# Kernel tuning notes

Hardware: AMD Instinct MI355X
Metric: run time of the kernel (lower is better)

## Reference

```python
import jax, jax.numpy as jnp
import numpy as np
import math

N_HEAD = 16
N_EMBD = 1024
HEAD_DIM = N_EMBD // N_HEAD
B, T = 2, 2048


def setup_inputs() -> dict:
    key = jax.random.key(0)
    k1, k2, k3 = jax.random.split(key, 3)
    scale = 0.02
    x = jax.random.normal(k1, (B, T, N_EMBD), dtype=jnp.float32)
    W_attn = jax.random.normal(k2, (N_EMBD, 3 * N_EMBD), dtype=jnp.float32) * scale
    b_attn = jnp.zeros((3 * N_EMBD,), dtype=jnp.float32)
    W_proj = jax.random.normal(k3, (N_EMBD, N_EMBD), dtype=jnp.float32) * scale
    b_proj = jnp.zeros((N_EMBD,), dtype=jnp.float32)
    return {"x": x, "W_attn": W_attn, "b_attn": b_attn, "W_proj": W_proj, "b_proj": b_proj}


def reference(x, W_attn, b_attn, W_proj, b_proj):
    b, t, c = x.shape
    qkv = x @ W_attn + b_attn                      # [B,T,3C]
    q, k, v = jnp.split(qkv, 3, axis=-1)
    # [B,T,C] -> [B,H,T,D]
    def heads(z):
        return z.reshape(b, t, N_HEAD, HEAD_DIM).transpose(0, 2, 1, 3)
    q, k, v = heads(q), heads(k), heads(v)
    att = jnp.einsum('bhqd,bhkd->bhqk', q, k) * (1.0 / math.sqrt(HEAD_DIM))
    causal = jnp.tril(jnp.ones((t, t), dtype=bool))  # [T,T]
    att = jnp.where(causal[None, None], att, -jnp.inf)
    att = jax.nn.softmax(att, axis=-1)
    y = jnp.einsum('bhqk,bhkd->bhqd', att, v)      # [B,H,T,D]
    y = y.transpose(0, 2, 1, 3).reshape(b, t, c)   # [B,T,C]
    return y @ W_proj + b_proj
```

## Files before the change

### kernel.cpp

```cpp
#include <hip/hip_runtime.h>
#include <hip/hip_bf16.h>


typedef __bf16 bf16_t;
typedef __bf16 bf16x8 __attribute__((ext_vector_type(8)));
typedef float f32x4 __attribute__((ext_vector_type(4)));
typedef unsigned short ushort_t;

#define QSCALE 0.18033688011f

__device__ __forceinline__ void glds16(const bf16_t* g, ushort_t* l) {
  __builtin_amdgcn_global_load_lds(
      (const __attribute__((address_space(1))) unsigned int*)g,
      (__attribute__((address_space(3))) unsigned int*)l, 16, 0, 0);
}

__global__ __launch_bounds__(256) void prep_kernel(
    const float* __restrict__ x, const float* __restrict__ W_attn,
    const float* __restrict__ W_proj, ushort_t* __restrict__ Xb,
    ushort_t* __restrict__ WtA, ushort_t* __restrict__ WtP) {
  const int bid = blockIdx.x, tid = threadIdx.x;
  if (bid < 4096) {
    int i = bid * 256 + tid;
    float4 v = ((const float4*)x)[i];
    ushort4 o;
    o.x = __builtin_bit_cast(unsigned short, (bf16_t)v.x);
    o.y = __builtin_bit_cast(unsigned short, (bf16_t)v.y);
    o.z = __builtin_bit_cast(unsigned short, (bf16_t)v.z);
    o.w = __builtin_bit_cast(unsigned short, (bf16_t)v.w);
    ((ushort4*)Xb)[i] = o;
    return;
  }
  __shared__ ushort_t tile[32][33];
  const float* in;
  ushort_t* out;
  int C, bx, by;
  if (bid < 4096 + 3072) { int idx = bid - 4096; in = W_attn; out = WtA; C = 3072; bx = idx % 96; by = idx / 96; }
  else                   { int idx = bid - 7168; in = W_proj; out = WtP; C = 1024; bx = idx % 32; by = idx / 32; }
  const int tx = tid & 31, ty = tid >> 5;
  int cbase = bx * 32, rbase = by * 32;
#pragma unroll
  for (int i = ty; i < 32; i += 8)
    tile[i][tx] = __builtin_bit_cast(
        unsigned short, (bf16_t)in[(size_t)(rbase + i) * C + cbase + tx]);
  __syncthreads();
#pragma unroll
  for (int i = ty; i < 32; i += 8)
    out[(size_t)(cbase + i) * 1024 + rbase + tx] = tile[tx][i];
}

__device__ __forceinline__ void gemm128_mainloop(
    const bf16_t* __restrict__ A, const bf16_t* __restrict__ Bt, int K,
    int mtile, int ntile, ushort_t* As, ushort_t* Bs, f32x4 acc[4][4]) {
  const int tid  = threadIdx.x;
  const int lane = tid & 63, wave = tid >> 6;
  const int l15  = lane & 15, quad = lane >> 4;
  const int wrow = (wave >> 1) * 64, wcol = (wave & 1) * 64;
  const int lr = lane >> 2;
  const int lc = (((lane & 3) ^ ((lr >> 1) & 3)) * 8);
  const bf16_t* Ap = A + (size_t)(mtile + wave * 32 + lr) * K + lc;
  const bf16_t* Bp = Bt + (size_t)(ntile + wave * 32 + lr) * K + lc;
  const int rsw = (quad ^ ((l15 >> 1) & 3)) * 8;
  ushort_t* Asw = As + wave * 32 * 32;
  ushort_t* Bsw = Bs + wave * 32 * 32;
  for (int kb = 0; kb < K; kb += 32) {
    __syncthreads();
#pragma unroll
    for (int c = 0; c < 2; c++) {
      glds16(Ap + (size_t)(c * 16) * K + kb, Asw + c * 16 * 32);
      glds16(Bp + (size_t)(c * 16) * K + kb, Bsw + c * 16 * 32);
    }
    __syncthreads();
    bf16x8 af[4], bfr[4];
#pragma unroll
    for (int i = 0; i < 4; i++)
      af[i] = *(const bf16x8*)&As[(wrow + i * 16 + l15) * 32 + rsw];
#pragma unroll
    for (int j = 0; j < 4; j++)
      bfr[j] = *(const bf16x8*)&Bs[(wcol + j * 16 + l15) * 32 + rsw];
#pragma unroll
    for (int i = 0; i < 4; i++)
#pragma unroll
      for (int j = 0; j < 4; j++)
        acc[i][j] = __builtin_amdgcn_mfma_f32_16x16x32_bf16(af[i], bfr[j], acc[i][j], 0, 0, 0);
  }
}

__global__ __launch_bounds__(256) void qkv_gemm_kernel(
    const bf16_t* __restrict__ X, const bf16_t* __restrict__ WtA,
    const float* __restrict__ bias, bf16_t* __restrict__ Qd,
    bf16_t* __restrict__ Kd, bf16_t* __restrict__ Vtd) {
  __shared__ ushort_t As[128 * 32];
  __shared__ ushort_t Bs[128 * 32];
  const int mtile = blockIdx.x * 128, ntile = blockIdx.y * 128;
  f32x4 acc[4][4] = {};
  gemm128_mainloop(X, WtA, 1024, mtile, ntile, As, Bs, acc);
  const int tid = threadIdx.x, lane = tid & 63, wave = tid >> 6;
  const int l15 = lane & 15, quad = lane >> 4;
  const int wrow = (wave >> 1) * 64, wcol = (wave & 1) * 64;
#pragma unroll
  for (int j = 0; j < 4; j++) {
    int n = ntile + wcol + j * 16 + l15;
    float bv = bias[n];
    int sec = n >> 10, cc = n & 1023, h = cc >> 6, d = cc & 63;
    float sv = (sec == 0) ? QSCALE : 1.0f;
#pragma unroll
    for (int i = 0; i < 4; i++) {
#pragma unroll
      for (int r = 0; r < 4; r++) {
        int m = mtile + wrow + i * 16 + quad * 4 + r;
        int b = m >> 11, t = m & 2047;
        size_t bh = (size_t)(b * 16 + h);
        bf16_t v = (bf16_t)((acc[i][j][r] + bv) * sv);
        if (sec == 0)      Qd[(bh * 2048 + t) * 64 + d] = v;
        else if (sec == 1) Kd[(bh * 2048 + t) * 64 + d] = v;
        else               Vtd[(bh * 64 + d) * 2048 + t] = v;
      }
    }
  }
}

__global__ __launch_bounds__(512) void attn_kernel(
    const bf16_t* __restrict__ Q, const bf16_t* __restrict__ K,
    const bf16_t* __restrict__ Vt, bf16_t* __restrict__ Y) {
  __shared__ ushort_t Ks[2][4096];
  __shared__ ushort_t Vs[2][4096];
  __shared__ ushort_t Ps[8][16 * 40];
  const int bh = blockIdx.y;
  const int qt = (blockIdx.y < 16) ? (15 - (int)blockIdx.x) : (int)blockIdx.x;
  const int tid = threadIdx.x, wave = tid >> 6, lane = tid & 63;
  const int l15 = lane & 15, quad = lane >> 4;
  const bf16_t* Qh = Q + (size_t)bh * 2048 * 64;
  const bf16_t* Kh = K + (size_t)bh * 2048 * 64;
  const bf16_t* Vh = Vt + (size_t)bh * 64 * 2048;
  const int b = bh >> 4, h = bh & 15;
  const int qw = qt * 128 + wave * 16;
  const int nkt = 2 * qt + 2;

  bf16x8 qa[2];
#pragma unroll
  for (int kc = 0; kc < 2; kc++)
    qa[kc] = *(const bf16x8*)(Qh + (size_t)(qw + l15) * 64 + kc * 32 + quad * 8);

  f32x4 o[4] = {};
  float lpart[4] = {};
  const int rsw = (quad ^ ((l15 >> 1) & 3)) * 8;

  const int lr4 = lane >> 2;
  const int csw = ((lane & 3) ^ ((lr4 >> 1) & 3)) * 8;
  const bool isK = wave < 4;
  const int sw = isK ? wave : wave - 4;
  const int rbase = (sw & 1) * 32;
  const bf16_t* gp0;
  size_t rowstep;
  if (isK) { gp0 = Kh + (size_t)(rbase + lr4) * 64 + (sw >> 1) * 32 + csw;  rowstep = 64; }
  else     { gp0 = Vh + (size_t)(rbase + lr4) * 2048 + (sw >> 1) * 32 + csw; rowstep = 2048; }
  const size_t kstep = isK ? (size_t)64 * 64 : 64;
  ushort_t* dst0 = (isK ? Ks[0] : Vs[0]) + (sw >> 1) * 2048 + rbase * 32;
  ushort_t* dst1 = (isK ? Ks[1] : Vs[1]) + (sw >> 1) * 2048 + rbase * 32;

#pragma unroll
  for (int c = 0; c < 2; c++)
    glds16(gp0 + (size_t)(c * 16) * rowstep, dst0 + c * 512);

  f32x4 zz = {0.f, 0.f, 0.f, 0.f};
  for (int kt = 0; kt < nkt; kt++) {
    const int cur = kt & 1;
    __syncthreads();
    if (kt + 1 < nkt) {
      ushort_t* nd = cur ? dst0 : dst1;
#pragma unroll
      for (int c = 0; c < 2; c++)
        glds16(gp0 + (size_t)(kt + 1) * kstep + (size_t)(c * 16) * rowstep, nd + c * 512);
    }
#pragma unroll
    for (int h32 = 0; h32 < 2; h32++) {
      const int kb32 = kt * 64 + h32 * 32;
      if (kb32 > qw + 15) break;
      bf16x8 kb[2][2];
#pragma unroll
      for (int bn = 0; bn < 2; bn++)
#pragma unroll
        for (int kc = 0; kc < 2; kc++)
          kb[bn][kc] = *(const bf16x8*)&Ks[cur][kc * 2048 + (h32 * 32 + bn * 16 + l15) * 32 + rsw];
      f32x4 s[2];
#pragma unroll
      for (int bn = 0; bn < 2; bn++) {
        f32x4 t0 = __builtin_amdgcn_mfma_f32_16x16x32_bf16(qa[0], kb[bn][0], zz, 0, 0, 0);
        s[bn] = __builtin_amdgcn_mfma_f32_16x16x32_bf16(qa[1], kb[bn][1], t0, 0, 0, 0);
      }
      const bool dg = (kb32 + 31 > qw);
#pragma unroll
      for (int r = 0; r < 4; r++) {
        int row = qw + quad * 4 + r;
        float v0 = s[0][r];
        float v1 = s[1][r];
        if (dg) {
          int c0 = kb32 + l15;
          if (c0 > row) v0 = -1e5f;
          if (c0 + 16 > row) v1 = -1e5f;
        }
        float p0 = __builtin_amdgcn_exp2f(v0);
        float p1 = __builtin_amdgcn_exp2f(v1);
        lpart[r] += p0 + p1;
        int prow = (quad * 4 + r) * 40;
        Ps[wave][prow + l15]      = __builtin_bit_cast(unsigned short, (bf16_t)p0);
        Ps[wave][prow + 16 + l15] = __builtin_bit_cast(unsigned short, (bf16_t)p1);
      }
      bf16x8 vb[4];
#pragma unroll
      for (int ns = 0; ns < 4; ns++)
        vb[ns] = *(const bf16x8*)&Vs[cur][h32 * 2048 + (ns * 16 + l15) * 32 + rsw];
      __asm__ volatile("" ::: "memory");
      bf16x8 pa = *(const bf16x8*)&Ps[wave][l15 * 40 + quad * 8];
#pragma unroll
      for (int ns = 0; ns < 4; ns++)
        o[ns] = __builtin_amdgcn_mfma_f32_16x16x32_bf16(pa, vb[ns], o[ns], 0, 0, 0);
    }
  }
#pragma unroll
  for (int r = 0; r < 4; r++) {
    float l = lpart[r];
#pragma unroll
    for (int off = 1; off < 16; off <<= 1) l += __shfl_xor(l, off);
    float inv_l = 1.0f / fmaxf(l, 1e-30f);
    int t = qw + quad * 4 + r;
#pragma unroll
    for (int ns = 0; ns < 4; ns++) {
      int c = h * 64 + ns * 16 + l15;
      Y[((size_t)(b * 2048 + t)) * 1024 + c] = (bf16_t)(o[ns][r] * inv_l);
    }
  }
}

__global__ __launch_bounds__(256) void proj_gemm_kernel(
    const bf16_t* __restrict__ Yb, const bf16_t* __restrict__ WtP,
    const float* __restrict__ bias, float* __restrict__ out) {
  __shared__ ushort_t As[128 * 32];
  __shared__ ushort_t Bs[64 * 32];
  const int tid = threadIdx.x;
  const int lane = tid & 63, wave = tid >> 6;
  const int l15 = lane & 15, quad = lane >> 4;
  const int wrow = (wave >> 1) * 64, wcol = (wave & 1) * 32;
  const int mtile = blockIdx.x * 128, ntile = blockIdx.y * 64;
  const int K = 1024;
  const int lr = lane >> 2;
  const int lc = (((lane & 3) ^ ((lr >> 1) & 3)) * 8);
  const bf16_t* Ap = Yb + (size_t)(mtile + wave * 32 + lr) * K + lc;
  const bf16_t* Bp = WtP + (size_t)(ntile + wave * 16 + lr) * K + lc;
  const int rsw = (quad ^ ((l15 >> 1) & 3)) * 8;
  ushort_t* Asw = As + wave * 32 * 32;
  ushort_t* Bsw = Bs + wave * 16 * 32;
  f32x4 acc[4][2] = {};
  for (int kb = 0; kb < K; kb += 32) {
    __syncthreads();
    glds16(Ap + kb, Asw);
    glds16(Ap + (size_t)16 * K + kb, Asw + 16 * 32);
    glds16(Bp + kb, Bsw);
    __syncthreads();
    bf16x8 af[4], bfr[2];
#pragma unroll
    for (int i = 0; i < 4; i++)
      af[i] = *(const bf16x8*)&As[(wrow + i * 16 + l15) * 32 + rsw];
#pragma unroll
    for (int j = 0; j < 2; j++)
      bfr[j] = *(const bf16x8*)&Bs[(wcol + j * 16 + l15) * 32 + rsw];
#pragma unroll
    for (int i = 0; i < 4; i++)
#pragma unroll
      for (int j = 0; j < 2; j++)
        acc[i][j] = __builtin_amdgcn_mfma_f32_16x16x32_bf16(af[i], bfr[j], acc[i][j], 0, 0, 0);
  }
  const int tid2 = threadIdx.x;
  (void)tid2;
#pragma unroll
  for (int j = 0; j < 2; j++) {
    int n = ntile + wcol + j * 16 + l15;
    float bv = bias[n];
#pragma unroll
    for (int i = 0; i < 4; i++) {
#pragma unroll
      for (int r = 0; r < 4; r++) {
        int m = mtile + wrow + i * 16 + quad * 4 + r;
        out[(size_t)m * 1024 + n] = acc[i][j][r] + bv;
      }
    }
  }
}

extern "C" void kernel_launch(void* const* d_in, const int* in_sizes, int n_in,
                              void* d_out, int out_size, void* d_ws, size_t ws_size,
                              hipStream_t stream) {
  const float* x      = (const float*)d_in[0];
  const float* W_attn = (const float*)d_in[1];
  const float* b_attn = (const float*)d_in[2];
  const float* W_proj = (const float*)d_in[3];
  const float* b_proj = (const float*)d_in[4];
  float* out = (float*)d_out;

  bf16_t* ws  = (bf16_t*)d_ws;
  bf16_t* WtA = ws;
  bf16_t* WtP = WtA + (size_t)3072 * 1024;
  bf16_t* Xb  = WtP + (size_t)1024 * 1024;
  bf16_t* Qb  = Xb + (size_t)4194304;
  bf16_t* Kb  = Qb + (size_t)4194304;
  bf16_t* Vtb = Kb + (size_t)4194304;
  bf16_t* Yb  = Vtb + (size_t)4194304;

  prep_kernel<<<8192, 256, 0, stream>>>(x, W_attn, W_proj,
      (ushort_t*)Xb, (ushort_t*)WtA, (ushort_t*)WtP);
  qkv_gemm_kernel<<<dim3(32, 24), 256, 0, stream>>>(Xb, WtA, b_attn, Qb, Kb, Vtb);
  attn_kernel<<<dim3(16, 32), 512, 0, stream>>>(Qb, Kb, Vtb, Yb);
  proj_gemm_kernel<<<dim3(32, 16), 256, 0, stream>>>(Yb, WtP, b_proj, out);
}
```

Before: 176.7 us.

## Double-buffer LDS tiles in QKV and projection GEMMs; vectorize V-transpose stores

Both GEMM main loops now use two LDS buffers. The next K-slice is prefetched with global_load_lds while MFMAs run on the current slice, which cuts the per-iteration barriers from two to one. The QKV epilogue is specialized per output section, and the transposed V stores are written as 4-element vector stores instead of scattered scalar ones. This doubles LDS use per block and relies on the single trailing barrier plus the compiler's waitcnt to order the async LDS loads correctly.

```diff
diff --git a/kernel.cpp b/kernel.cpp
--- a/kernel.cpp
+++ b/kernel.cpp
@@ -61,28 +61,36 @@
   const bf16_t* Ap = A + (size_t)(mtile + wave * 32 + lr) * K + lc;
   const bf16_t* Bp = Bt + (size_t)(ntile + wave * 32 + lr) * K + lc;
   const int rsw = (quad ^ ((l15 >> 1) & 3)) * 8;
-  ushort_t* Asw = As + wave * 32 * 32;
-  ushort_t* Bsw = Bs + wave * 32 * 32;
-  for (int kb = 0; kb < K; kb += 32) {
-    __syncthreads();
-#pragma unroll
-    for (int c = 0; c < 2; c++) {
-      glds16(Ap + (size_t)(c * 16) * K + kb, Asw + c * 16 * 32);
-      glds16(Bp + (size_t)(c * 16) * K + kb, Bsw + c * 16 * 32);
-    }
-    __syncthreads();
+  const int woff = wave * 32 * 32;
+#pragma unroll
+  for (int c = 0; c < 2; c++) {
+    glds16(Ap + (size_t)(c * 16) * K, As + woff + c * 16 * 32);
+    glds16(Bp + (size_t)(c * 16) * K, Bs + woff + c * 16 * 32);
+  }
+  __syncthreads();
+  const int nkb = K >> 5;
+  for (int t = 0; t < nkb; t++) {
+    const int cur = t & 1, nxt = cur ^ 1;
+    if (t + 1 < nkb) {
+#pragma unroll
+      for (int c = 0; c < 2; c++) {
+        glds16(Ap + (size_t)(c * 16) * K + (t + 1) * 32, As + nxt * 4096 + woff + c * 16 * 32);
+        glds16(Bp + (size_t)(c * 16) * K + (t + 1) * 32, Bs + nxt * 4096 + woff + c * 16 * 32);
+      }
+    }
     bf16x8 af[4], bfr[4];
 #pragma unroll
     for (int i = 0; i < 4; i++)
-      af[i] = *(const bf16x8*)&As[(wrow + i * 16 + l15) * 32 + rsw];
+      af[i] = *(const bf16x8*)&As[cur * 4096 + (wrow + i * 16 + l15) * 32 + rsw];
 #pragma unroll
     for (int j = 0; j < 4; j++)
-      bfr[j] = *(const bf16x8*)&Bs[(wcol + j * 16 + l15) * 32 + rsw];
+      bfr[j] = *(const bf16x8*)&Bs[cur * 4096 + (wcol + j * 16 + l15) * 32 + rsw];
 #pragma unroll
     for (int i = 0; i < 4; i++)
 #pragma unroll
       for (int j = 0; j < 4; j++)
         acc[i][j] = __builtin_amdgcn_mfma_f32_16x16x32_bf16(af[i], bfr[j], acc[i][j], 0, 0, 0);
+    __syncthreads();
   }
 }
 
@@ -90,31 +98,50 @@
     const bf16_t* __restrict__ X, const bf16_t* __restrict__ WtA,
     const float* __restrict__ bias, bf16_t* __restrict__ Qd,
     bf16_t* __restrict__ Kd, bf16_t* __restrict__ Vtd) {
-  __shared__ ushort_t As[128 * 32];
-  __shared__ ushort_t Bs[128 * 32];
+  __shared__ ushort_t As[2 * 128 * 32];
+  __shared__ ushort_t Bs[2 * 128 * 32];
   const int mtile = blockIdx.x * 128, ntile = blockIdx.y * 128;
   f32x4 acc[4][4] = {};
   gemm128_mainloop(X, WtA, 1024, mtile, ntile, As, Bs, acc);
   const int tid = threadIdx.x, lane = tid & 63, wave = tid >> 6;
   const int l15 = lane & 15, quad = lane >> 4;
   const int wrow = (wave >> 1) * 64, wcol = (wave & 1) * 64;
+  const int sec = ntile >> 10;
+  const int b = mtile >> 11;
+  if (sec == 2) {
+#pragma unroll
+    for (int j = 0; j < 4; j++) {
+      int n = ntile + wcol + j * 16 + l15;
+      float bv = bias[n];
+      int cc = n & 1023, h = cc >> 6, d = cc & 63;
+      size_t bh = (size_t)(b * 16 + h);
+#pragma unroll
+      for (int i = 0; i < 4; i++) {
+        int tbase = (mtile & 2047) + wrow + i * 16 + quad * 4;
+        ushort4 o4;
+        o4.x = __builtin_bit_cast(unsigned short, (bf16_t)(acc[i][j][0] + bv));
+        o4.y = __builtin_bit_cast(unsigned short, (bf16_t)(acc[i][j][1] + bv));
+        o4.z = __builtin_bit_cast(unsigned short, (bf16_t)(acc[i][j][2] + bv));
+        o4.w = __builtin_bit_cast(unsigned short, (bf16_t)(acc[i][j][3] + bv));
+        *(ushort4*)&Vtd[(bh * 64 + d) * 2048 + tbase] = o4;
+      }
+    }
+    return;
+  }
+  const float sv = (sec == 0) ? QSCALE : 1.0f;
+  bf16_t* Od = (sec == 0) ? Qd : Kd;
 #pragma unroll
   for (int j = 0; j < 4; j++) {
     int n = ntile + wcol + j * 16 + l15;
     float bv = bias[n];
-    int sec = n >> 10, cc = n & 1023, h = cc >> 6, d = cc & 63;
-    float sv = (sec == 0) ? QSCALE : 1.0f;
+    int cc = n & 1023, h = cc >> 6, d = cc & 63;
+    size_t bh = (size_t)(b * 16 + h);
 #pragma unroll
     for (int i = 0; i < 4; i++) {
 #pragma unroll
       for (int r = 0; r < 4; r++) {
-        int m = mtile + wrow + i * 16 + quad * 4 + r;
-        int b = m >> 11, t = m & 2047;
-        size_t bh = (size_t)(b * 16 + h);
-        bf16_t v = (bf16_t)((acc[i][j][r] + bv) * sv);
-        if (sec == 0)      Qd[(bh * 2048 + t) * 64 + d] = v;
-        else if (sec == 1) Kd[(bh * 2048 + t) * 64 + d] = v;
-        else               Vtd[(bh * 64 + d) * 2048 + t] = v;
+        int t = (mtile & 2047) + wrow + i * 16 + quad * 4 + r;
+        Od[(bh * 2048 + t) * 64 + d] = (bf16_t)((acc[i][j][r] + bv) * sv);
       }
     }
   }
@@ -236,8 +263,8 @@
 __global__ __launch_bounds__(256) void proj_gemm_kernel(
     const bf16_t* __restrict__ Yb, const bf16_t* __restrict__ WtP,
     const float* __restrict__ bias, float* __restrict__ out) {
-  __shared__ ushort_t As[128 * 32];
-  __shared__ ushort_t Bs[64 * 32];
+  __shared__ ushort_t As[2 * 128 * 32];
+  __shared__ ushort_t Bs[2 * 64 * 32];
   const int tid = threadIdx.x;
   const int lane = tid & 63, wave = tid >> 6;
   const int l15 = lane & 15, quad = lane >> 4;
@@ -249,30 +276,33 @@
   const bf16_t* Ap = Yb + (size_t)(mtile + wave * 32 + lr) * K + lc;
   const bf16_t* Bp = WtP + (size_t)(ntile + wave * 16 + lr) * K + lc;
   const int rsw = (quad ^ ((l15 >> 1) & 3)) * 8;
-  ushort_t* Asw = As + wave * 32 * 32;
-  ushort_t* Bsw = Bs + wave * 16 * 32;
+  const int wa = wave * 32 * 32, wb = wave * 16 * 32;
   f32x4 acc[4][2] = {};
-  for (int kb = 0; kb < K; kb += 32) {
-    __syncthreads();
-    glds16(Ap + kb, Asw);
-    glds16(Ap + (size_t)16 * K + kb, Asw + 16 * 32);
-    glds16(Bp + kb, Bsw);
-    __syncthreads();
+  glds16(Ap, As + wa);
+  glds16(Ap + (size_t)16 * K, As + wa + 16 * 32);
+  glds16(Bp, Bs + wb);
+  __syncthreads();
+  for (int t = 0; t < 32; t++) {
+    const int cur = t & 1, nxt = cur ^ 1;
+    if (t + 1 < 32) {
+      glds16(Ap + (t + 1) * 32, As + nxt * 4096 + wa);
+      glds16(Ap + (size_t)16 * K + (t + 1) * 32, As + nxt * 4096 + wa + 16 * 32);
+      glds16(Bp + (t + 1) * 32, Bs + nxt * 2048 + wb);
+    }
     bf16x8 af[4], bfr[2];
 #pragma unroll
     for (int i = 0; i < 4; i++)
-      af[i] = *(const bf16x8*)&As[(wrow + i * 16 + l15) * 32 + rsw];
+      af[i] = *(const bf16x8*)&As[cur * 4096 + (wrow + i * 16 + l15) * 32 + rsw];
 #pragma unroll
     for (int j = 0; j < 2; j++)
-      bfr[j] = *(const bf16x8*)&Bs[(wcol + j * 16 + l15) * 32 + rsw];
+      bfr[j] = *(const bf16x8*)&Bs[cur * 2048 + (wcol + j * 16 + l15) * 32 + rsw];
 #pragma unroll
     for (int i = 0; i < 4; i++)
 #pragma unroll
       for (int j = 0; j < 2; j++)
         acc[i][j] = __builtin_amdgcn_mfma_f32_16x16x32_bf16(af[i], bfr[j], acc[i][j], 0, 0, 0);
-  }
-  const int tid2 = threadIdx.x;
-  (void)tid2;
+    __syncthreads();
+  }
 #pragma unroll
   for (int j = 0; j < 2; j++) {
     int n = ntile + wcol + j * 16 + l15;
```

Result: slower. 194.5 us (+10.0%).
